# Kernel optimization log

Measured on AMD Instinct MI355X. Metric: run time of the kernel, lower is better.

## Reference

```python
import jax, jax.numpy as jnp
import numpy as np

EMBED_DIM = 256
NUM_HEADS = 8
TEMPERATURE = 10000.0
SCALE = 100.0
EPS = 1e-5


def setup_inputs() -> dict:
    key = jax.random.key(0)
    k1, k2, k3 = jax.random.split(key, 3)
    B, N, H, Wd = 1, 300, 24, 80
    # depths in a realistic positive range
    predict_depth = jax.random.uniform(k1, (B, N), dtype=jnp.float32) * 60.0
    depth_map = jax.random.uniform(k2, (B, H, Wd), dtype=jnp.float32) * 60.0
    # nn.Linear(embed_dim, num_heads): store as (in, out)
    W = jax.random.normal(k3, (EMBED_DIM, NUM_HEADS), dtype=jnp.float32) * 0.05
    b = jnp.zeros((NUM_HEADS,), dtype=jnp.float32)
    return {"predict_depth": predict_depth, "depth_map": depth_map, "W": W, "b": b}


def reference(predict_depth, depth_map, W, b):
    B, H, Wd = depth_map.shape
    HW = H * Wd
    N = predict_depth.shape[1]
    dm = depth_map.reshape(B, HW)
    pd = jax.nn.relu(predict_depth)
    # depth log-ratio: (B, N, HW)
    delta = jnp.log((pd[:, :, None] + EPS) / (dm[:, None, :] + EPS))
    # sine/cos embedding with interleaved sin/cos per frequency -> (B, N, HW, 256)
    dim_t = TEMPERATURE ** (jnp.arange(EMBED_DIM // 2, dtype=jnp.float32) * 2.0 / EMBED_DIM)
    pos = delta[..., None] * SCALE / dim_t  # (B, N, HW, 128)
    pos = jnp.stack((jnp.sin(pos), jnp.cos(pos)), axis=-1).reshape(B, N, HW, EMBED_DIM)
    # computed under torch.no_grad() in the original
    pos = jax.lax.stop_gradient(pos)
    # Linear(256 -> num_heads) + ReLU
    out = jax.nn.relu(pos @ W + b)  # (B, N, HW, heads)
    # permute(0,3,1,2).flatten(0,1) -> (B*heads, N, HW)
    out = jnp.transpose(out, (0, 3, 1, 2)).reshape(B * NUM_HEADS, N, HW)
    return out
```

## Files before the change

### kernel.cpp

```cpp
#include <hip/hip_runtime.h>
#include <hip/hip_bf16.h>

#define NPTS   300
#define HW_SZ  1920
#define TOTAL  (NPTS * HW_SZ)
#define NCOL   2400
#define L2T128 0.10381025293350249f
#define KREVL2 3.9923601817f

#define BM   128
#define BN   64
#define LDK2 136
#define SNP  132
#define WPP  132
#define MT   15
#define CT   38

typedef __attribute__((ext_vector_type(8))) short short8;
typedef __attribute__((ext_vector_type(4))) float floatx4;

union frag_u { unsigned u[4]; short8 s; };

__device__ __forceinline__ unsigned pk_bf16(float lo, float hi) {
    return __builtin_amdgcn_perm(__float_as_uint(hi) + 0x8000u,
                                 __float_as_uint(lo) + 0x8000u,
                                 0x07060302u);
}
__device__ __forceinline__ float blo(unsigned u) { return __uint_as_float(u << 16); }
__device__ __forceinline__ float bhi(unsigned u) { return __uint_as_float(u & 0xffff0000u); }

__global__ __launch_bounds__(256, 3) void dre_v12(const float* __restrict__ pd,
                                                  const float* __restrict__ dm,
                                                  const float* __restrict__ W,
                                                  const float* __restrict__ b,
                                                  float* __restrict__ out)
{
    __shared__ float    kfr[128];
    __shared__ float    ldm[BM];
    __shared__ float    snq[8 * SNP];
    __shared__ float    cnq[8 * SNP];
    __shared__ unsigned wpk[8 * WPP];
    __shared__ unsigned short BsP[BN * LDK2];
    __shared__ unsigned short BsQ[BN * LDK2];

    const int tid = threadIdx.x;
    const int m0  = blockIdx.x * BM;
    const int c0  = blockIdx.y * BN;
    const int n0  = c0 >> 3;

    if (tid < 128)      kfr[tid] = exp2f(KREVL2 - (float)tid * L2T128);
    else                ldm[tid - 128 + 64] = __logf(dm[m0 + tid - 64] + 1e-5f);
    if (tid < 64)       ldm[tid] = __logf(dm[m0 + tid] + 1e-5f);
    {
        const int h = tid & 7, i0 = (tid >> 3) * 4;
        unsigned pk[4];
#pragma unroll
        for (int j = 0; j < 4; ++j)
            pk[j] = pk_bf16(W[(i0 + j) * 16 + h], W[(i0 + j) * 16 + 8 + h]);
        *(uint4*)&wpk[h * WPP + i0] = make_uint4(pk[0], pk[1], pk[2], pk[3]);
    }
    {
        const int nl = tid >> 5, i0 = (tid & 31) * 4;
        const int nn = n0 + nl;
        const float pv = (nn < NPTS) ? pd[nn] : 0.0f;
        const float lp = __logf(fmaxf(pv, 0.0f) + 1e-5f);
        float s[4], c[4];
#pragma unroll
        for (int j = 0; j < 4; ++j) {
            const float a = exp2f(KREVL2 - (float)(i0 + j) * L2T128) * lp;
            s[j] = __builtin_amdgcn_sinf(a);
            c[j] = __builtin_amdgcn_cosf(a);
        }
        *(float4*)&snq[nl * SNP + i0] = make_float4(s[0], s[1], s[2], s[3]);
        *(float4*)&cnq[nl * SNP + i0] = make_float4(c[0], c[1], c[2], c[3]);
    }
    __syncthreads();

    {
        const int bcr = tid >> 2, q = tid & 3;
        const int bnl = bcr >> 3, bh = bcr & 7;
#pragma unroll
        for (int half = 0; half < 2; ++half) {
            const int ib0 = q * 32 + half * 16;
            unsigned pp[8], qq[8];
#pragma unroll
            for (int g = 0; g < 4; ++g) {
                const int i4 = ib0 + g * 4;
                const float4 s4 = *(const float4*)&snq[bnl * SNP + i4];
                const float4 c4 = *(const float4*)&cnq[bnl * SNP + i4];
                const uint4  w4 = *(const uint4*)&wpk[bh * WPP + i4];
                const float ws0 = blo(w4.x), wc0 = bhi(w4.x);
                const float ws1 = blo(w4.y), wc1 = bhi(w4.y);
                const float ws2 = blo(w4.z), wc2 = bhi(w4.z);
                const float ws3 = blo(w4.w), wc3 = bhi(w4.w);
                const float P0 = ws0*s4.x + wc0*c4.x, Q0 = wc0*s4.x - ws0*c4.x;
                const float P1 = ws1*s4.y + wc1*c4.y, Q1 = wc1*s4.y - ws1*c4.y;
                const float P2 = ws2*s4.z + wc2*c4.z, Q2 = wc2*s4.z - ws2*c4.z;
                const float P3 = ws3*s4.w + wc3*c4.w, Q3 = wc3*s4.w - ws3*c4.w;
                pp[2*g] = pk_bf16(P0, P1);  pp[2*g+1] = pk_bf16(P2, P3);
                qq[2*g] = pk_bf16(Q0, Q1);  qq[2*g+1] = pk_bf16(Q2, Q3);
            }
            *(uint4*)&BsP[bcr * LDK2 + ib0]     = make_uint4(pp[0], pp[1], pp[2], pp[3]);
            *(uint4*)&BsP[bcr * LDK2 + ib0 + 8] = make_uint4(pp[4], pp[5], pp[6], pp[7]);
            *(uint4*)&BsQ[bcr * LDK2 + ib0]     = make_uint4(qq[0], qq[1], qq[2], qq[3]);
            *(uint4*)&BsQ[bcr * LDK2 + ib0 + 8] = make_uint4(qq[4], qq[5], qq[6], qq[7]);
        }
    }
    __syncthreads();

    const int w = tid >> 6, lane = tid & 63, quad = lane >> 4, l16 = lane & 15;
    const float ldr0 = ldm[w * 32 + l16];
    const float ldr1 = ldm[w * 32 + 16 + l16];

    floatx4 acc[2][4];
#pragma unroll
    for (int mi = 0; mi < 2; ++mi)
#pragma unroll
        for (int nf = 0; nf < 4; ++nf) acc[mi][nf] = (floatx4){0.f, 0.f, 0.f, 0.f};

#pragma unroll
    for (int ib = 0; ib < 2; ++ib) {
        frag_u cf[2][2], sf[2][2];
#pragma unroll
        for (int ks = 0; ks < 2; ++ks) {
            const int kb = ib * 64 + ks * 32 + quad * 8;
            const float4 f0 = *(const float4*)&kfr[kb];
            const float4 f1 = *(const float4*)&kfr[kb + 4];
            const float fr[8] = {f0.x, f0.y, f0.z, f0.w, f1.x, f1.y, f1.z, f1.w};
            float s0[8], c0v[8], s1[8], c1v[8];
#pragma unroll
            for (int j = 0; j < 8; ++j) {
                const float a0 = fr[j] * ldr0;
                const float a1 = fr[j] * ldr1;
                s0[j]  = __builtin_amdgcn_sinf(a0);
                c0v[j] = __builtin_amdgcn_cosf(a0);
                s1[j]  = __builtin_amdgcn_sinf(a1);
                c1v[j] = __builtin_amdgcn_cosf(a1);
            }
#pragma unroll
            for (int r = 0; r < 4; ++r) {
                cf[0][ks].u[r] = pk_bf16(c0v[2*r], c0v[2*r+1]);
                sf[0][ks].u[r] = pk_bf16(s0[2*r],  s0[2*r+1]);
                cf[1][ks].u[r] = pk_bf16(c1v[2*r], c1v[2*r+1]);
                sf[1][ks].u[r] = pk_bf16(s1[2*r],  s1[2*r+1]);
            }
        }
#pragma unroll
        for (int ks = 0; ks < 2; ++ks) {
            const int koff = ib * 64 + ks * 32 + quad * 8;
#pragma unroll
            for (int nf = 0; nf < 4; ++nf) {
                short8 bp = *(const short8*)&BsP[(nf * 16 + l16) * LDK2 + koff];
                acc[0][nf] = __builtin_amdgcn_mfma_f32_16x16x32_bf16(cf[0][ks].s, bp, acc[0][nf], 0, 0, 0);
                acc[1][nf] = __builtin_amdgcn_mfma_f32_16x16x32_bf16(cf[1][ks].s, bp, acc[1][nf], 0, 0, 0);
                short8 bq = *(const short8*)&BsQ[(nf * 16 + l16) * LDK2 + koff];
                acc[0][nf] = __builtin_amdgcn_mfma_f32_16x16x32_bf16(sf[0][ks].s, bq, acc[0][nf], 0, 0, 0);
                acc[1][nf] = __builtin_amdgcn_mfma_f32_16x16x32_bf16(sf[1][ks].s, bq, acc[1][nf], 0, 0, 0);
            }
        }
    }

    const float bias = b[lane & 7];
#pragma unroll
    for (int mi = 0; mi < 2; ++mi) {
#pragma unroll
        for (int nf = 0; nf < 4; ++nf) {
            const int c = c0 + nf * 16 + l16;
            if (c < NCOL) {
                const int n = c >> 3, h = c & 7;
                const int hw = m0 + w * 32 + mi * 16 + quad * 4;
                floatx4 v = acc[mi][nf];
                v.x = fmaxf(v.x + bias, 0.0f);
                v.y = fmaxf(v.y + bias, 0.0f);
                v.z = fmaxf(v.z + bias, 0.0f);
                v.w = fmaxf(v.w + bias, 0.0f);
                *(floatx4*)(out + (size_t)h * TOTAL + (size_t)n * HW_SZ + hw) = v;
            }
        }
    }
}

extern "C" void kernel_launch(void* const* d_in, const int* in_sizes, int n_in,
                              void* d_out, int out_size, void* d_ws, size_t ws_size,
                              hipStream_t stream) {
    const float* pd = (const float*)d_in[0];
    const float* dm = (const float*)d_in[1];
    const float* W  = (const float*)d_in[2];
    const float* b  = (const float*)d_in[3];
    float* out = (float*)d_out;

    dre_v12<<<dim3(MT, CT), 256, 0, stream>>>(pd, dm, W, b, out);
}
```

Before: 71.86 us.

## Compute A-fragment trig in registers before the barrier, drop kfr/ldm shared arrays

Each thread now loads its own depth-map values and takes their logs directly, instead of going through a shared ldm array. It also computes the frequency factors with exp2f inline rather than reading a shared kfr table. All sin/cos A-fragments for both k-halves are built before the first barrier, so this trig work can overlap the B-tile construction and remove a shared-memory round trip. The cost is higher register pressure from holding 16 packed fragments, which may force spills or lower occupancy under the launch bound of 3 blocks.

```diff
diff --git a/kernel.cpp b/kernel.cpp
--- a/kernel.cpp
+++ b/kernel.cpp
@@ -29,28 +29,27 @@
 __device__ __forceinline__ float blo(unsigned u) { return __uint_as_float(u << 16); }
 __device__ __forceinline__ float bhi(unsigned u) { return __uint_as_float(u & 0xffff0000u); }
 
-__global__ __launch_bounds__(256, 3) void dre_v12(const float* __restrict__ pd,
+__global__ __launch_bounds__(256, 3) void dre_v15(const float* __restrict__ pd,
                                                   const float* __restrict__ dm,
                                                   const float* __restrict__ W,
                                                   const float* __restrict__ b,
                                                   float* __restrict__ out)
 {
-    __shared__ float    kfr[128];
-    __shared__ float    ldm[BM];
     __shared__ float    snq[8 * SNP];
     __shared__ float    cnq[8 * SNP];
     __shared__ unsigned wpk[8 * WPP];
     __shared__ unsigned short BsP[BN * LDK2];
     __shared__ unsigned short BsQ[BN * LDK2];
 
-    const int tid = threadIdx.x;
-    const int m0  = blockIdx.x * BM;
-    const int c0  = blockIdx.y * BN;
-    const int n0  = c0 >> 3;
+    const int tid  = threadIdx.x;
+    const int m0   = blockIdx.x * BM;
+    const int c0   = blockIdx.y * BN;
+    const int n0   = c0 >> 3;
+    const int w    = tid >> 6, lane = tid & 63, quad = lane >> 4, l16 = lane & 15;
 
-    if (tid < 128)      kfr[tid] = exp2f(KREVL2 - (float)tid * L2T128);
-    else                ldm[tid - 128 + 64] = __logf(dm[m0 + tid - 64] + 1e-5f);
-    if (tid < 64)       ldm[tid] = __logf(dm[m0 + tid] + 1e-5f);
+    const float dv0 = dm[m0 + w * 32 + l16];
+    const float dv1 = dm[m0 + w * 32 + 16 + l16];
+
     {
         const int h = tid & 7, i0 = (tid >> 3) * 4;
         unsigned pk[4];
@@ -74,6 +73,35 @@
         *(float4*)&snq[nl * SNP + i0] = make_float4(s[0], s[1], s[2], s[3]);
         *(float4*)&cnq[nl * SNP + i0] = make_float4(c[0], c[1], c[2], c[3]);
     }
+
+    const float ldr0 = __logf(dv0 + 1e-5f);
+    const float ldr1 = __logf(dv1 + 1e-5f);
+    frag_u cf[2][2][2], sf[2][2][2];
+#pragma unroll
+    for (int ib = 0; ib < 2; ++ib) {
+#pragma unroll
+        for (int ks = 0; ks < 2; ++ks) {
+            const int kb = ib * 64 + ks * 32 + quad * 8;
+            float s0[8], c0v[8], s1[8], c1v[8];
+#pragma unroll
+            for (int j = 0; j < 8; ++j) {
+                const float krev = exp2f(KREVL2 - (float)(kb + j) * L2T128);
+                const float a0 = krev * ldr0, a1 = krev * ldr1;
+                s0[j]  = __builtin_amdgcn_sinf(a0);
+                c0v[j] = __builtin_amdgcn_cosf(a0);
+                s1[j]  = __builtin_amdgcn_sinf(a1);
+                c1v[j] = __builtin_amdgcn_cosf(a1);
+            }
+#pragma unroll
+            for (int r = 0; r < 4; ++r) {
+                cf[ib][ks][0].u[r] = pk_bf16(c0v[2*r], c0v[2*r+1]);
+                sf[ib][ks][0].u[r] = pk_bf16(s0[2*r],  s0[2*r+1]);
+                cf[ib][ks][1].u[r] = pk_bf16(c1v[2*r], c1v[2*r+1]);
+                sf[ib][ks][1].u[r] = pk_bf16(s1[2*r],  s1[2*r+1]);
+            }
+        }
+    }
+
     __syncthreads();
 
     {
@@ -108,10 +136,6 @@
     }
     __syncthreads();
 
-    const int w = tid >> 6, lane = tid & 63, quad = lane >> 4, l16 = lane & 15;
-    const float ldr0 = ldm[w * 32 + l16];
-    const float ldr1 = ldm[w * 32 + 16 + l16];
-
     floatx4 acc[2][4];
 #pragma unroll
     for (int mi = 0; mi < 2; ++mi)
@@ -120,42 +144,17 @@
 
 #pragma unroll
     for (int ib = 0; ib < 2; ++ib) {
-        frag_u cf[2][2], sf[2][2];
-#pragma unroll
-        for (int ks = 0; ks < 2; ++ks) {
-            const int kb = ib * 64 + ks * 32 + quad * 8;
-            const float4 f0 = *(const float4*)&kfr[kb];
-            const float4 f1 = *(const float4*)&kfr[kb + 4];
-            const float fr[8] = {f0.x, f0.y, f0.z, f0.w, f1.x, f1.y, f1.z, f1.w};
-            float s0[8], c0v[8], s1[8], c1v[8];
-#pragma unroll
-            for (int j = 0; j < 8; ++j) {
-                const float a0 = fr[j] * ldr0;
-                const float a1 = fr[j] * ldr1;
-                s0[j]  = __builtin_amdgcn_sinf(a0);
-                c0v[j] = __builtin_amdgcn_cosf(a0);
-                s1[j]  = __builtin_amdgcn_sinf(a1);
-                c1v[j] = __builtin_amdgcn_cosf(a1);
-            }
-#pragma unroll
-            for (int r = 0; r < 4; ++r) {
-                cf[0][ks].u[r] = pk_bf16(c0v[2*r], c0v[2*r+1]);
-                sf[0][ks].u[r] = pk_bf16(s0[2*r],  s0[2*r+1]);
-                cf[1][ks].u[r] = pk_bf16(c1v[2*r], c1v[2*r+1]);
-                sf[1][ks].u[r] = pk_bf16(s1[2*r],  s1[2*r+1]);
-            }
-        }
 #pragma unroll
         for (int ks = 0; ks < 2; ++ks) {
             const int koff = ib * 64 + ks * 32 + quad * 8;
 #pragma unroll
             for (int nf = 0; nf < 4; ++nf) {
                 short8 bp = *(const short8*)&BsP[(nf * 16 + l16) * LDK2 + koff];
-                acc[0][nf] = __builtin_amdgcn_mfma_f32_16x16x32_bf16(cf[0][ks].s, bp, acc[0][nf], 0, 0, 0);
-                acc[1][nf] = __builtin_amdgcn_mfma_f32_16x16x32_bf16(cf[1][ks].s, bp, acc[1][nf], 0, 0, 0);
+                acc[0][nf] = __builtin_amdgcn_mfma_f32_16x16x32_bf16(cf[ib][ks][0].s, bp, acc[0][nf], 0, 0, 0);
+                acc[1][nf] = __builtin_amdgcn_mfma_f32_16x16x32_bf16(cf[ib][ks][1].s, bp, acc[1][nf], 0, 0, 0);
                 short8 bq = *(const short8*)&BsQ[(nf * 16 + l16) * LDK2 + koff];
-                acc[0][nf] = __builtin_amdgcn_mfma_f32_16x16x32_bf16(sf[0][ks].s, bq, acc[0][nf], 0, 0, 0);
-                acc[1][nf] = __builtin_amdgcn_mfma_f32_16x16x32_bf16(sf[1][ks].s, bq, acc[1][nf], 0, 0, 0);
+                acc[0][nf] = __builtin_amdgcn_mfma_f32_16x16x32_bf16(sf[ib][ks][0].s, bq, acc[0][nf], 0, 0, 0);
+                acc[1][nf] = __builtin_amdgcn_mfma_f32_16x16x32_bf16(sf[ib][ks][1].s, bq, acc[1][nf], 0, 0, 0);
             }
         }
     }
@@ -189,5 +188,5 @@
     const float* b  = (const float*)d_in[3];
     float* out = (float*)d_out;
 
-    dre_v12<<<dim3(MT, CT), 256, 0, stream>>>(pd, dm, W, b, out);
+    dre_v15<<<dim3(MT, CT), 256, 0, stream>>>(pd, dm, W, b, out);
 }
```

Result: no change. 72.87 us (+1.4%).
